# Kernel tuning notes

Hardware: AMD Instinct MI355X
Metric: run time of the kernel (lower is better)

Reference implementation:

```python
import jax, jax.numpy as jnp
import numpy as np
from math import sqrt

D_MODEL = 1024
HEADS = 16
D_K = D_MODEL // HEADS
NEG = -1e9


def setup_inputs() -> dict:
    key = jax.random.key(0)
    ks = jax.random.split(key, 8)
    bs, s, d = 2, 2048, D_MODEL
    inp = {
        "k": jax.random.normal(ks[0], (bs, s, d), jnp.float32),
        "v": jax.random.normal(ks[1], (bs, s, d), jnp.float32),
        "q": jax.random.normal(ks[2], (bs, s, d), jnp.float32),
        "mask": jax.random.randint(ks[3], (bs, s, 1), 0, 2).astype(jnp.int64),
        # torch nn.Linear weights: y = x @ W.T, W is [out, in]
        "Wq": jax.random.normal(ks[4], (d, d), jnp.float32) / sqrt(d),
        "Wk": jax.random.normal(ks[5], (d, d), jnp.float32) / sqrt(d),
        "Wv": jax.random.normal(ks[6], (d, d), jnp.float32) / sqrt(d),
        "Wo": jax.random.normal(ks[7], (d, d), jnp.float32) / sqrt(d),
    }
    return inp


def reference(k, v, q, mask, Wq, Wk, Wv, Wo):
    bs, s_k, d = k.shape
    s_q = q.shape[1]
    h, d_k = HEADS, D_K
    # linear projections (no bias), then split heads -> [bs, h, s, d_k]
    kh = (k @ Wk.T).reshape(bs, s_k, h, d_k).transpose(0, 2, 1, 3)
    vh = (v @ Wv.T).reshape(bs, s_k, h, d_k).transpose(0, 2, 1, 3)
    qh = (q @ Wq.T).reshape(bs, s_q, h, d_k).transpose(0, 2, 1, 3)
    # scaled dot-product scores [bs, h, s_q, s_k]
    scores = jnp.einsum("bhqd,bhkd->bhqk", qh, kh) / sqrt(d_k)
    # mask [bs, s_k, 1] -> [bs, 1, 1, s_k], masked positions get -1e9
    m = mask[:, None].transpose(0, 1, 3, 2)  # [bs,1,1,s_k]
    scores = jnp.where(m == 0, NEG, scores)
    probs = jax.nn.softmax(scores, axis=-1)  # dropout is identity (eval)
    attn = jnp.einsum("bhqk,bhkd->bhqd", probs, vh)
    attn_concat = attn.transpose(0, 2, 1, 3).reshape(bs, s_q, d)
    return attn_concat @ Wo.T
```

## Files before the change

kernel.cpp:

```cpp
#include <hip/hip_runtime.h>

typedef __bf16 bf16x8 __attribute__((ext_vector_type(8)));
typedef float f32x4 __attribute__((ext_vector_type(4)));

#define BS 2
#define SEQ 2048
#define DM 1024
#define NH 16
#define DKH 64
#define GM 4096
#define GN 1024
#define GK 1024
#define NEGV (-1e9f)

#define OFF_XQ 0u
#define OFF_XK 4194304u
#define OFF_XV 8388608u
#define OFF_WQ 12582912u
#define OFF_WK 13631488u
#define OFF_WV 14680064u
#define OFF_WO 15728640u
#define OFF_QH 16777216u
#define OFF_KC 20971520u
#define OFF_VT 25165824u
#define OFF_AT OFF_XQ

#if __has_builtin(__builtin_amdgcn_exp2f)
#define EXP2(x) __builtin_amdgcn_exp2f(x)
#else
static __device__ __forceinline__ float EXP2(float x) {
    float r;
    asm volatile("v_exp_f32 %0, %1" : "=v"(r) : "v"(x));
    return r;
}
#endif

__device__ __forceinline__ unsigned cvt_pk(float lo, float hi) {
    unsigned r;
    asm volatile("v_cvt_pk_bf16_f32 %0, %1, %2" : "=v"(r) : "v"(lo), "v"(hi));
    return r;
}

__device__ __forceinline__ unsigned short f2b(float f) {
    unsigned u = __builtin_bit_cast(unsigned, f);
    u += 0x7fffu + ((u >> 16) & 1u);
    return (unsigned short)(u >> 16);
}

typedef const __attribute__((address_space(1))) unsigned int* gas_t;
typedef __attribute__((address_space(3))) unsigned int* las_t;

__device__ __forceinline__ void gload_lds16(const ushort* g, ushort* l) {
    __builtin_amdgcn_global_load_lds((gas_t)(const void*)g, (las_t)(void*)l, 16, 0, 0);
}

#define BARRIER() __builtin_amdgcn_s_barrier()
#define VMCNT(n) asm volatile("s_waitcnt vmcnt(" #n ")" ::: "memory")

__global__ __launch_bounds__(256)
void cvt_scan(const float* __restrict__ q, const float* __restrict__ k,
              const float* __restrict__ v, const float* __restrict__ wq,
              const float* __restrict__ wk, const float* __restrict__ wv,
              const float* __restrict__ wo, ushort* __restrict__ ws,
              const int* __restrict__ mask, int* __restrict__ cpos,
              int* __restrict__ mbuf)
{
    const int tid = threadIdx.x;
    if (blockIdx.y == 7) {
        if (blockIdx.x >= 2) return;
        const int b = blockIdx.x;
        const int* mp = mask + (size_t)b * SEQ;
        const int lane = tid & 63, w = tid >> 6;
        int vv[8];
        int cnt = 0;
#pragma unroll
        for (int j = 0; j < 8; ++j) { vv[j] = mp[tid * 8 + j]; cnt += (vv[j] != 0); }
        int inc = cnt;
#pragma unroll
        for (int d = 1; d < 64; d <<= 1) {
            int t = __shfl_up(inc, d);
            if (lane >= d) inc += t;
        }
        __shared__ int wsum[4];
        if (lane == 63) wsum[w] = inc;
        __syncthreads();
        int base = inc - cnt;
        for (int i = 0; i < w; ++i) base += wsum[i];
        int c = base;
        int* ob = cpos + (size_t)b * SEQ;
#pragma unroll
        for (int j = 0; j < 8; ++j) {
            ob[tid * 8 + j] = (vv[j] != 0) ? c : -1;
            c += (vv[j] != 0);
        }
        if (tid == 255) mbuf[b] = base + cnt;
        return;
    }
    const float* src; unsigned n; unsigned dst;
    switch (blockIdx.y) {
        case 0: src = q;  n = 4194304u; dst = OFF_XQ; break;
        case 1: src = k;  n = 4194304u; dst = OFF_XK; break;
        case 2: src = v;  n = 4194304u; dst = OFF_XV; break;
        case 3: src = wq; n = 1048576u; dst = OFF_WQ; break;
        case 4: src = wk; n = 1048576u; dst = OFF_WK; break;
        case 5: src = wv; n = 1048576u; dst = OFF_WV; break;
        default: src = wo; n = 1048576u; dst = OFF_WO; break;
    }
    unsigned i = (blockIdx.x * 256u + tid) * 8u;
    if (i >= n) return;
    float4 f0 = *(const float4*)(src + i);
    float4 f1 = *(const float4*)(src + i + 4);
    uint4 o;
    o.x = cvt_pk(f0.x, f0.y);
    o.y = cvt_pk(f0.z, f0.w);
    o.z = cvt_pk(f1.x, f1.y);
    o.w = cvt_pk(f1.z, f1.w);
    *(uint4*)(ws + dst + i) = o;
}

__global__ __launch_bounds__(512)
void gemm256(const ushort* __restrict__ Abase, const ushort* __restrict__ Bbase,
             ushort* __restrict__ wsbase, const int* __restrict__ cpos)
{
    __shared__ __align__(16) ushort lA[2][2][8192];
    __shared__ __align__(16) ushort lB[2][2][8192];

    const unsigned z = blockIdx.z;
    const ushort* A  = Abase + (size_t)z * (GM * GK);
    const ushort* Bw = Bbase + (size_t)z * (GN * GK);
    const float scale = (z == 0) ? 0.125f * 1.44269504088896f : 1.0f;

    const int tid = threadIdx.x;
    const int lane = tid & 63, wid = tid >> 6;
    const int wr = wid >> 2, wc = wid & 3;
    const int lr = lane & 15, lg = lane >> 4;
    const int srow8 = lane >> 3, scol = lane & 7;

    const int lin = blockIdx.y * 4 + blockIdx.x;
    const int xcd = lin & 7, kidx = lin >> 3;
    const int m0 = (xcd * 2 + (kidx >> 2)) * 256;
    const int n0 = (kidx & 3) * 256;

    f32x4 acc[8][4] = {};
    bf16x8 aq[4][2], aq2[4][2], b01[2][2], b23[2][2];

#define STAGE_A(s, h, t)                                                          \
    _Pragma("unroll") for (int c = 0; c < 2; ++c) {                               \
        int rih = (wid * 2 + c) * 8 + srow8;                                      \
        gload_lds16(A + (size_t)(m0 + (h) * 128 + rih) * GK + (t) * 64 +          \
                        ((scol ^ (rih & 7)) * 8),                                 \
                    &lA[s][h][(wid * 2 + c) * 512]);                              \
    }
#define STAGE_B(s, h, t)                                                          \
    _Pragma("unroll") for (int c = 0; c < 2; ++c) {                               \
        int rih = (wid * 2 + c) * 8 + srow8;                                      \
        gload_lds16(Bw + (size_t)(n0 + (h) * 128 + rih) * GK + (t) * 64 +         \
                         ((scol ^ (rih & 7)) * 8),                                \
                    &lB[s][h][(wid * 2 + c) * 512]);                              \
    }
#define LDA_FRAG(dst, s, ibase)                                                   \
    _Pragma("unroll") for (int i2 = 0; i2 < 4; ++i2)                              \
    _Pragma("unroll") for (int kk = 0; kk < 2; ++kk) {                            \
        int row = ((ibase) + i2) * 16 + lr;                                       \
        dst[i2][kk] = *(const bf16x8*)&lA[s][wr][row * 64 +                       \
                          (((kk * 4 + lg) ^ (row & 7)) * 8)];                     \
    }
#define LDB_FRAG(dst, s, jbase)                                                   \
    _Pragma("unroll") for (int j2 = 0; j2 < 2; ++j2)                              \
    _Pragma("unroll") for (int kk = 0; kk < 2; ++kk) {                            \
        int row = (wc & 1) * 64 + ((jbase) + j2) * 16 + lr;                       \
        dst[j2][kk] = *(const bf16x8*)&lB[s][wc >> 1][row * 64 +                  \
                          (((kk * 4 + lg) ^ (row & 7)) * 8)];                     \
    }
#define MMA_Q(ibase, jbase, av, bv)                                               \
    __builtin_amdgcn_s_setprio(1);                                                \
    _Pragma("unroll") for (int i2 = 0; i2 < 4; ++i2)                              \
    _Pragma("unroll") for (int j2 = 0; j2 < 2; ++j2)                              \
    _Pragma("unroll") for (int kk = 0; kk < 2; ++kk)                              \
        acc[(ibase) + i2][(jbase) + j2] = __builtin_amdgcn_mfma_f32_16x16x32_bf16(\
            av[i2][kk], bv[j2][kk], acc[(ibase) + i2][(jbase) + j2], 0, 0, 0);    \
    __builtin_amdgcn_s_setprio(0);

    STAGE_B(0, 0, 0); STAGE_B(0, 1, 0); STAGE_A(0, 0, 0); STAGE_A(0, 1, 0);
    STAGE_B(1, 0, 1); STAGE_B(1, 1, 1); STAGE_A(1, 0, 1); STAGE_A(1, 1, 1);
    VMCNT(8);
    BARRIER();

    for (int it = 0; it < 7; ++it) {
        const int t2 = 2 * it + 2, t3 = 2 * it + 3;
        LDA_FRAG(aq, 0, 0); LDB_FRAG(b01, 0, 0); LDB_FRAG(b23, 0, 2);
        BARRIER();
        MMA_Q(0, 0, aq, b01); MMA_Q(0, 2, aq, b23);
        BARRIER();
        LDA_FRAG(aq2, 0, 4);
        STAGE_B(0, 0, t2); STAGE_B(0, 1, t2); STAGE_A(0, 0, t2); STAGE_A(0, 1, t2);
        VMCNT(8);
        BARRIER();
        MMA_Q(4, 2, aq2, b23); MMA_Q(4, 0, aq2, b01);
        BARRIER();
        LDA_FRAG(aq, 1, 0); LDB_FRAG(b01, 1, 0); LDB_FRAG(b23, 1, 2);
        BARRIER();
        MMA_Q(0, 0, aq, b01); MMA_Q(0, 2, aq, b23);
        BARRIER();
        LDA_FRAG(aq2, 1, 4);
        STAGE_B(1, 0, t3); STAGE_B(1, 1, t3); STAGE_A(1, 0, t3); STAGE_A(1, 1, t3);
        VMCNT(8);
        BARRIER();
        MMA_Q(4, 2, aq2, b23); MMA_Q(4, 0, aq2, b01);
        BARRIER();
    }

    LDA_FRAG(aq, 0, 0); LDB_FRAG(b01, 0, 0); LDB_FRAG(b23, 0, 2);
    BARRIER();
    MMA_Q(0, 0, aq, b01); MMA_Q(0, 2, aq, b23);
    BARRIER();
    LDA_FRAG(aq2, 0, 4);
    VMCNT(0);
    BARRIER();
    MMA_Q(4, 2, aq2, b23); MMA_Q(4, 0, aq2, b01);
    BARRIER();
    LDA_FRAG(aq, 1, 0); LDB_FRAG(b01, 1, 0); LDB_FRAG(b23, 1, 2);
    BARRIER();
    MMA_Q(0, 0, aq, b01); MMA_Q(0, 2, aq, b23);
    BARRIER();
    LDA_FRAG(aq2, 1, 4);
    BARRIER();
    MMA_Q(4, 2, aq2, b23); MMA_Q(4, 0, aq2, b01);
    BARRIER();

    ushort* qh  = wsbase + OFF_QH;
    ushort* kc  = wsbase + OFF_KC;
    ushort* vtp = wsbase + OFF_VT;
#pragma unroll
    for (int i = 0; i < 8; ++i) {
#pragma unroll
        for (int r = 0; r < 4; ++r) {
            int row = m0 + wr * 128 + i * 16 + lg * 4 + r;
            int b = row >> 11, s = row & 2047;
            if (z == 0) {
#pragma unroll
                for (int j = 0; j < 4; ++j) {
                    int col = n0 + wc * 64 + j * 16 + lr;
                    qh[(((size_t)b * NH + (col >> 6)) * SEQ + s) * DKH + (col & 63)] =
                        f2b(acc[i][j][r] * scale);
                }
            } else {
                int c = cpos[b * SEQ + s];
                if (c >= 0) {
                    if (z == 1) {
#pragma unroll
                        for (int j = 0; j < 4; ++j) {
                            int col = n0 + wc * 64 + j * 16 + lr;
                            kc[(((size_t)b * NH + (col >> 6)) * SEQ + c) * DKH + (col & 63)] =
                                f2b(acc[i][j][r]);
                        }
                    } else {
                        int vt = (c & ~63) | ((c & 15) * 4 + ((c >> 4) & 3));
#pragma unroll
                        for (int j = 0; j < 4; ++j) {
                            int col = n0 + wc * 64 + j * 16 + lr;
                            vtp[(((size_t)b * NH + (col >> 6)) * DKH + (col & 63)) * SEQ + vt] =
                                f2b(acc[i][j][r]);
                        }
                    }
                }
            }
        }
    }
#undef STAGE_A
#undef STAGE_B
#undef LDA_FRAG
#undef LDB_FRAG
#undef MMA_Q
}

__global__ __launch_bounds__(256)
void gemm_bt(const ushort* __restrict__ A, const ushort* __restrict__ Bw,
             float* __restrict__ of)
{
    __shared__ __align__(16) ushort lA[128 * 64];
    __shared__ __align__(16) ushort lB[128 * 64];

    const int tid = threadIdx.x;
    const int lane = tid & 63, wid = tid >> 6;
    const int wr = wid >> 1, wc = wid & 1;
    const int lr = lane & 15, lg = lane >> 4;
    const int lin = blockIdx.y * 8 + blockIdx.x;
    const int swz = (lin & 7) * 32 + (lin >> 3);
    const int m0 = (swz >> 3) * 128, n0 = (swz & 7) * 128;
    const int srow = wid * 32 + (lane >> 3);
    const int scol = (lane & 7) * 8;

    f32x4 acc[4][4] = {};

    for (int k0 = 0; k0 < GK; k0 += 64) {
        __syncthreads();
#pragma unroll
        for (int p = 0; p < 4; ++p) {
            gload_lds16(A + (size_t)(m0 + srow + p * 8) * GK + k0 + scol,
                        &lA[(wid * 32 + p * 8) * 64]);
            gload_lds16(Bw + (size_t)(n0 + srow + p * 8) * GK + k0 + scol,
                        &lB[(wid * 32 + p * 8) * 64]);
        }
        __syncthreads();
#pragma unroll
        for (int kk = 0; kk < 2; ++kk) {
            bf16x8 af[4], bfr[4];
#pragma unroll
            for (int i = 0; i < 4; ++i) {
                af[i]  = *(const bf16x8*)(&lA[(wr * 64 + i * 16 + lr) * 64 + kk * 32 + lg * 8]);
                bfr[i] = *(const bf16x8*)(&lB[(wc * 64 + i * 16 + lr) * 64 + kk * 32 + lg * 8]);
            }
#pragma unroll
            for (int i = 0; i < 4; ++i)
#pragma unroll
                for (int j = 0; j < 4; ++j)
                    acc[i][j] = __builtin_amdgcn_mfma_f32_16x16x32_bf16(af[i], bfr[j], acc[i][j], 0, 0, 0);
        }
    }

#pragma unroll
    for (int i = 0; i < 4; ++i)
#pragma unroll
        for (int j = 0; j < 4; ++j) {
            int col = n0 + wc * 64 + j * 16 + lr;
#pragma unroll
            for (int r = 0; r < 4; ++r) {
                int row = m0 + wr * 64 + i * 16 + lg * 4 + r;
                of[(size_t)row * GN + col] = acc[i][j][r];
            }
        }
}

__global__ __launch_bounds__(256)
void attn_kernel(ushort* __restrict__ ws, const int* __restrict__ mbuf)
{
    const int bid = blockIdx.x;
    const int qt = bid & 15;
    const int h  = (bid >> 4) & 15;
    const int b  = bid >> 8;
    const int bh = b * NH + h;

    const ushort* Qp = ws + OFF_QH + (size_t)bh * (SEQ * DKH);
    const ushort* Kc = ws + OFF_KC + (size_t)bh * (SEQ * DKH);
    const ushort* VT = ws + OFF_VT + (size_t)bh * (DKH * SEQ);
    ushort* At = ws + OFF_AT;

    const int mb = mbuf[b];
    const int nt = (mb + 63) >> 6;

    __shared__ __align__(16) ushort lK[3][64 * 64];
    __shared__ __align__(16) ushort lV[3][64 * 64];
    __shared__ __align__(16) ushort lP[4][32][72];

    const int tid = threadIdx.x;
    const int lane = tid & 63, wid = tid >> 6;
    const int lr = lane & 15, lg = lane >> 4;
    ushort* lPw = &lP[wid][0][0];

    const int srow = wid * 16 + (lane >> 3);
    const int sg = lane & 7;

    const int qrow0 = qt * 128 + wid * 32;
    bf16x8 qf[2][2];
#pragma unroll
    for (int fr = 0; fr < 2; ++fr)
#pragma unroll
        for (int kk = 0; kk < 2; ++kk)
            qf[fr][kk] = *(const bf16x8*)(Qp + (size_t)(qrow0 + fr * 16 + lr) * DKH + kk * 32 + lg * 8);

    f32x4 acc_o[2][4] = {};
    float lrun[2][4] = {};

    auto STAGE = [&](int buf, int kt) {
        const int kbase = kt * 64;
#pragma unroll
        for (int c = 0; c < 2; ++c) {
            int r = srow + c * 8;
            gload_lds16(Kc + (size_t)(kbase + r) * DKH + ((sg ^ (r & 7)) * 8),
                        &lK[buf][(wid * 16 + c * 8) * 64]);
            gload_lds16(VT + (size_t)r * SEQ + kbase + ((sg ^ (r & 7)) * 8),
                        &lV[buf][(wid * 16 + c * 8) * 64]);
        }
    };

    STAGE(0, 0);
    if (nt > 1) STAGE(1, 1);

    int slot = 0;
    for (int kt = 0; kt < nt; ++kt) {
        if (kt + 1 < nt) { VMCNT(4); } else { VMCNT(0); }
        BARRIER();
        if (kt + 2 < nt) {
            int s2 = slot + 2; if (s2 >= 3) s2 -= 3;
            STAGE(s2, kt + 2);
        }
        const ushort* lKc = lK[slot];
        const ushort* lVc = lV[slot];

        f32x4 s[2][4];
        __builtin_amdgcn_s_setprio(1);
#pragma unroll
        for (int fc = 0; fc < 4; ++fc) {
            int row = fc * 16 + lr;
            int sw = row & 7;
            bf16x8 kf0 = *(const bf16x8*)(lKc + row * 64 + ((lg ^ sw) * 8));
            bf16x8 kf1 = *(const bf16x8*)(lKc + row * 64 + (((4 + lg) ^ sw) * 8));
#pragma unroll
            for (int fr = 0; fr < 2; ++fr) {
                f32x4 t = {};
                t = __builtin_amdgcn_mfma_f32_16x16x32_bf16(qf[fr][0], kf0, t, 0, 0, 0);
                t = __builtin_amdgcn_mfma_f32_16x16x32_bf16(qf[fr][1], kf1, t, 0, 0, 0);
                s[fr][fc] = t;
            }
        }
        __builtin_amdgcn_s_setprio(0);

        if (kt == nt - 1) {
            const int kbase = kt * 64;
#pragma unroll
            for (int fc = 0; fc < 4; ++fc)
                if (kbase + fc * 16 + lr >= mb)
#pragma unroll
                    for (int fr = 0; fr < 2; ++fr)
                        s[fr][fc] = f32x4{NEGV, NEGV, NEGV, NEGV};
        }

#pragma unroll
        for (int fr = 0; fr < 2; ++fr)
#pragma unroll
            for (int r = 0; r < 4; ++r) {
                float p0 = EXP2(s[fr][0][r]), p1 = EXP2(s[fr][1][r]);
                float p2 = EXP2(s[fr][2][r]), p3 = EXP2(s[fr][3][r]);
                lrun[fr][r] += (p0 + p1) + (p2 + p3);
                uint2 pk;
                pk.x = cvt_pk(p0, p1);
                pk.y = cvt_pk(p2, p3);
                *(uint2*)(lPw + (fr * 16 + lg * 4 + r) * 72 + lr * 4) = pk;
            }

        __builtin_amdgcn_s_setprio(1);
#pragma unroll
        for (int kk = 0; kk < 2; ++kk) {
            bf16x8 pf[2];
#pragma unroll
            for (int fr = 0; fr < 2; ++fr)
                pf[fr] = *(const bf16x8*)(lPw + (fr * 16 + lr) * 72 + kk * 32 + lg * 8);
#pragma unroll
            for (int fc2 = 0; fc2 < 4; ++fc2) {
                int d = fc2 * 16 + lr;
                bf16x8 vf = *(const bf16x8*)(lVc + d * 64 + (((kk * 4 + lg) ^ (d & 7)) * 8));
#pragma unroll
                for (int fr = 0; fr < 2; ++fr)
                    acc_o[fr][fc2] = __builtin_amdgcn_mfma_f32_16x16x32_bf16(pf[fr], vf, acc_o[fr][fc2], 0, 0, 0);
            }
        }
        __builtin_amdgcn_s_setprio(0);

        ++slot; if (slot >= 3) slot -= 3;
    }

#pragma unroll
    for (int fr = 0; fr < 2; ++fr)
#pragma unroll
        for (int r = 0; r < 4; ++r) {
            float l = lrun[fr][r];
            l += __shfl_xor(l, 1);
            l += __shfl_xor(l, 2);
            l += __shfl_xor(l, 4);
            l += __shfl_xor(l, 8);
            float rl = 1.0f / l;
            int qrow = qrow0 + fr * 16 + lg * 4 + r;
#pragma unroll
            for (int fc2 = 0; fc2 < 4; ++fc2)
                At[((size_t)(b * SEQ) + qrow) * DM + h * DKH + fc2 * 16 + lr] =
                    f2b(acc_o[fr][fc2][r] * rl);
        }
}

extern "C" void kernel_launch(void* const* d_in, const int* in_sizes, int n_in,
                              void* d_out, int out_size, void* d_ws, size_t ws_size,
                              hipStream_t stream) {
    const float* kin = (const float*)d_in[0];
    const float* vin = (const float*)d_in[1];
    const float* qin = (const float*)d_in[2];
    const int*   msk = (const int*)d_in[3];
    const float* wq  = (const float*)d_in[4];
    const float* wk  = (const float*)d_in[5];
    const float* wv  = (const float*)d_in[6];
    const float* wo  = (const float*)d_in[7];
    ushort* ws = (ushort*)d_ws;
    float* out = (float*)d_out;
    int* cposb = (int*)d_out;
    int* mbuf = cposb + BS * SEQ;

    cvt_scan<<<dim3(2048, 8), 256, 0, stream>>>(qin, kin, vin, wq, wk, wv, wo,
                                                ws, msk, cposb, mbuf);
    gemm256<<<dim3(4, 16, 3), 512, 0, stream>>>(ws + OFF_XQ, ws + OFF_WQ, ws, cposb);
    attn_kernel<<<512, 256, 0, stream>>>(ws, mbuf);
    gemm_bt<<<dim3(8, 32), 256, 0, stream>>>(ws + OFF_AT, ws + OFF_WO, out);
}
```

Measured before the change: 120.4 us.

## Double-buffer output-projection GEMM LDS tiles with XOR swizzle and MFMA priority

The output-projection GEMM now keeps two LDS buffers and issues the next K-tile's global-to-LDS loads before computing on the current one, leaving one barrier per iteration instead of two. It XOR-swizzles the column chunk on both the store and read side to avoid LDS bank conflicts on the fragment reads. It also raises wave priority around the MFMA block. LDS use doubles, which may lower occupancy, and fragment registers double because both kk halves are loaded up front.

```diff
diff --git a/kernel.cpp b/kernel.cpp
--- a/kernel.cpp
+++ b/kernel.cpp
@@ -278,8 +278,8 @@
 void gemm_bt(const ushort* __restrict__ A, const ushort* __restrict__ Bw,
              float* __restrict__ of)
 {
-    __shared__ __align__(16) ushort lA[128 * 64];
-    __shared__ __align__(16) ushort lB[128 * 64];
+    __shared__ __align__(16) ushort lA[2][128 * 64];
+    __shared__ __align__(16) ushort lB[2][128 * 64];
 
     const int tid = threadIdx.x;
     const int lane = tid & 63, wid = tid >> 6;
@@ -288,35 +288,45 @@
     const int lin = blockIdx.y * 8 + blockIdx.x;
     const int swz = (lin & 7) * 32 + (lin >> 3);
     const int m0 = (swz >> 3) * 128, n0 = (swz & 7) * 128;
-    const int srow = wid * 32 + (lane >> 3);
-    const int scol = (lane & 7) * 8;
+    const int srow8 = lane >> 3, scol = lane & 7;
 
     f32x4 acc[4][4] = {};
-
-    for (int k0 = 0; k0 < GK; k0 += 64) {
+    bf16x8 af[2][4], bfr[2][4];
+
+#define OSTAGE(s, t)                                                               \
+    _Pragma("unroll") for (int p = 0; p < 4; ++p) {                                \
+        int r = wid * 32 + p * 8 + srow8;                                          \
+        gload_lds16(A + (size_t)(m0 + r) * GK + (t) * 64 + ((scol ^ (r & 7)) * 8), \
+                    &lA[s][(wid * 32 + p * 8) * 64]);                              \
+        gload_lds16(Bw + (size_t)(n0 + r) * GK + (t) * 64 + ((scol ^ (r & 7)) * 8),\
+                    &lB[s][(wid * 32 + p * 8) * 64]);                              \
+    }
+#define OLDX(s)                                                                    \
+    _Pragma("unroll") for (int kk = 0; kk < 2; ++kk)                               \
+    _Pragma("unroll") for (int i = 0; i < 4; ++i) {                                \
+        int ra = wr * 64 + i * 16 + lr;                                            \
+        af[kk][i] = *(const bf16x8*)&lA[s][ra * 64 + (((kk * 4 + lg) ^ (ra & 7)) * 8)];  \
+        int rb = wc * 64 + i * 16 + lr;                                            \
+        bfr[kk][i] = *(const bf16x8*)&lB[s][rb * 64 + (((kk * 4 + lg) ^ (rb & 7)) * 8)]; \
+    }
+#define OMMA()                                                                     \
+    __builtin_amdgcn_s_setprio(1);                                                 \
+    _Pragma("unroll") for (int kk = 0; kk < 2; ++kk)                               \
+    _Pragma("unroll") for (int i = 0; i < 4; ++i)                                  \
+    _Pragma("unroll") for (int j = 0; j < 4; ++j)                                  \
+        acc[i][j] = __builtin_amdgcn_mfma_f32_16x16x32_bf16(af[kk][i], bfr[kk][j], \
+                                                            acc[i][j], 0, 0, 0);   \
+    __builtin_amdgcn_s_setprio(0);
+
+    OSTAGE(0, 0);
+    __syncthreads();
+
+    for (int t = 0; t < 16; ++t) {
+        const int cur = t & 1;
+        if (t + 1 < 16) OSTAGE(cur ^ 1, t + 1);
+        OLDX(cur);
+        OMMA();
         __syncthreads();
-#pragma unroll
-        for (int p = 0; p < 4; ++p) {
-            gload_lds16(A + (size_t)(m0 + srow + p * 8) * GK + k0 + scol,
-                        &lA[(wid * 32 + p * 8) * 64]);
-            gload_lds16(Bw + (size_t)(n0 + srow + p * 8) * GK + k0 + scol,
-                        &lB[(wid * 32 + p * 8) * 64]);
-        }
-        __syncthreads();
-#pragma unroll
-        for (int kk = 0; kk < 2; ++kk) {
-            bf16x8 af[4], bfr[4];
-#pragma unroll
-            for (int i = 0; i < 4; ++i) {
-                af[i]  = *(const bf16x8*)(&lA[(wr * 64 + i * 16 + lr) * 64 + kk * 32 + lg * 8]);
-                bfr[i] = *(const bf16x8*)(&lB[(wc * 64 + i * 16 + lr) * 64 + kk * 32 + lg * 8]);
-            }
-#pragma unroll
-            for (int i = 0; i < 4; ++i)
-#pragma unroll
-                for (int j = 0; j < 4; ++j)
-                    acc[i][j] = __builtin_amdgcn_mfma_f32_16x16x32_bf16(af[i], bfr[j], acc[i][j], 0, 0, 0);
-        }
     }
 
 #pragma unroll
@@ -330,6 +340,9 @@
                 of[(size_t)row * GN + col] = acc[i][j][r];
             }
         }
+#undef OSTAGE
+#undef OLDX
+#undef OMMA
 }
 
 __global__ __launch_bounds__(256)
```

Result: no change. 120.1 us (-0.2%).
